# Optimization experiments

Hardware: AMD Instinct MI355X
Metric: run time of the kernel (lower is better)

The kernel has to match this reference:

```python
import jax, jax.numpy as jnp
import numpy as np

N, E, F, H, L, G, EMB, C = 50000, 600000, 128, 128, 4, 64, 64, 10
BN_EPS = 1e-5


def setup_inputs() -> dict:
    key = jax.random.key(0)
    k = lambda i: jax.random.fold_in(key, i)
    s = 0.05  # weight scale
    return {
        "x": jax.random.normal(k(0), (N, F), jnp.float32),
        "edge_index": jax.random.randint(k(1), (2, E), 0, N, jnp.int64),
        "batch": jnp.sort(jax.random.randint(k(2), (N,), 0, G, jnp.int64)),
        "emb": jax.random.normal(k(3), (G, EMB), jnp.float32),
        "eps": jnp.zeros((L,), jnp.float32),
        "W1": jax.random.normal(k(4), (L, F, H), jnp.float32) * s,
        "b1": jnp.zeros((L, H), jnp.float32),
        "W2": jax.random.normal(k(5), (L, H, H), jnp.float32) * s,
        "b2": jnp.zeros((L, H), jnp.float32),
        "gamma": jnp.ones((L, H), jnp.float32),
        "beta": jnp.zeros((L, H), jnp.float32),
        "lin1_w": jax.random.normal(k(6), (L * H + EMB, 2 * H), jnp.float32) * s,
        "lin1_b": jnp.zeros((2 * H,), jnp.float32),
        "lin2_w": jax.random.normal(k(7), (2 * H, H), jnp.float32) * s,
        "lin2_b": jnp.zeros((H,), jnp.float32),
        "lin4_w": jax.random.normal(k(8), (H, C), jnp.float32) * s,
        "lin4_b": jnp.zeros((C,), jnp.float32),
    }


def _gin_mlp(h, W1, b1, W2, b2, gamma, beta):
    # Linear -> ReLU -> Linear -> ReLU -> BatchNorm1d (batch stats)
    h = jax.nn.relu(h @ W1 + b1)
    h = jax.nn.relu(h @ W2 + b2)
    mean = jnp.mean(h, axis=0)
    var = jnp.var(h, axis=0)
    return (h - mean) * jax.lax.rsqrt(var + BN_EPS) * gamma + beta


def reference(x, edge_index, batch, emb, eps, W1, b1, W2, b2, gamma, beta,
              lin1_w, lin1_b, lin2_w, lin2_b, lin4_w, lin4_b):
    src, dst = edge_index[0], edge_index[1]
    xs = []
    for l in range(L):
        # GIN: MLP((1+eps)*x_i + sum_{j->i} x_j)  via gather + scatter-add
        agg = jax.ops.segment_sum(x[src], dst, num_segments=N)  # [N,H]
        x = _gin_mlp((1.0 + eps[l]) * x + agg,
                     W1[l], b1[l], W2[l], b2[l], gamma[l], beta[l])
        xs.append(x)
    h = jnp.concatenate(xs, axis=1)  # [N, L*H]
    # global mean pool per graph
    sums = jax.ops.segment_sum(h, batch, num_segments=G)  # [G, L*H]
    cnt = jax.ops.segment_sum(jnp.ones((N,), h.dtype), batch, num_segments=G)
    pooled = sums / jnp.maximum(cnt, 1.0)[:, None]
    z = jnp.concatenate([pooled, emb.reshape(G, -1)], axis=1)
    z = jax.nn.relu(z @ lin1_w + lin1_b)  # .relu() twice is idempotent
    # dropout p=0.5 skipped (eval mode); lin3 unused in original forward
    z = jax.nn.relu(z @ lin2_w + lin2_b)
    z = z @ lin4_w + lin4_b
    return jax.nn.log_softmax(z, axis=1)
```

## Files before the change

kernel.cpp:

```cpp
#include <hip/hip_runtime.h>
#include <cstdint>
#include <cstddef>

#define N_NODES 50000
#define N_EDGES 600000
#define NLAYER  4
#define NGRAPH  64
#define SCAN_NB 196
#define NBLK_MLP ((N_NODES + 127) / 128)
#define RED_B    ((NBLK_MLP + 12) / 13)

typedef unsigned int   u32;
typedef unsigned short u16;
typedef float f32x4  __attribute__((ext_vector_type(4)));
typedef short bf16x8 __attribute__((ext_vector_type(8)));

__device__ __forceinline__ float bf1(u16 u)  { return __uint_as_float(((u32)u) << 16); }
__device__ __forceinline__ float bflo(u32 u) { return __uint_as_float(u << 16); }
__device__ __forceinline__ float bfhi(u32 u) { return __uint_as_float(u & 0xffff0000u); }
__device__ __forceinline__ u16 f2bf(float f) {
    u32 x = __float_as_uint(f);
    u32 r = x + 0x7fffu + ((x >> 16) & 1u);
    return (u16)(r >> 16);
}
__device__ __forceinline__ u32 pack2(float a, float b) {
    return (u32)f2bf(a) | ((u32)f2bf(b) << 16);
}

__global__ __launch_bounds__(256) void cvt_x(const float2* __restrict__ x,
                                             u32* __restrict__ xbf) {
    int i = blockIdx.x * 256 + threadIdx.x;
    if (i < N_NODES * 64) { float2 v = x[i]; xbf[i] = pack2(v.x, v.y); }
}

__global__ __launch_bounds__(128) void cvt_w(const float* __restrict__ W1,
                                             const float* __restrict__ W2,
                                             short* __restrict__ W1t,
                                             short* __restrict__ W2t) {
    int l = blockIdx.y, n = blockIdx.x, k = threadIdx.x;
    const float* W = blockIdx.z ? W2 : W1;
    short* Wt      = blockIdx.z ? W2t : W1t;
    Wt[((size_t)l * 128 + n) * 128 + k] = (short)f2bf(W[((size_t)l * 128 + k) * 128 + n]);
}

__global__ void count_deg(const int* __restrict__ dst, int* __restrict__ deg) {
    int e = blockIdx.x * 256 + threadIdx.x;
    if (e < N_EDGES) atomicAdd(&deg[dst[e]], 1);
}

__global__ __launch_bounds__(256) void scan_l1(const int* __restrict__ deg,
                                               int* __restrict__ bscan,
                                               int* __restrict__ bsum) {
    __shared__ int sd[256];
    int tid = threadIdx.x;
    int i = blockIdx.x * 256 + tid;
    int v = (i < N_NODES) ? deg[i] : 0;
    sd[tid] = v; __syncthreads();
#pragma unroll
    for (int off = 1; off < 256; off <<= 1) {
        int t = (tid >= off) ? sd[tid - off] : 0;
        __syncthreads();
        sd[tid] += t; __syncthreads();
    }
    if (i < N_NODES) bscan[i] = sd[tid];
    if (tid == 255) bsum[blockIdx.x] = sd[255];
}

__global__ __launch_bounds__(256) void scan_l2(const int* __restrict__ bsum,
                                               int* __restrict__ boff) {
    __shared__ int sd[256];
    int tid = threadIdx.x;
    int v = (tid < SCAN_NB) ? bsum[tid] : 0;
    sd[tid] = v; __syncthreads();
#pragma unroll
    for (int off = 1; off < 256; off <<= 1) {
        int t = (tid >= off) ? sd[tid - off] : 0;
        __syncthreads();
        sd[tid] += t; __syncthreads();
    }
    if (tid < SCAN_NB) boff[tid] = sd[tid] - v;
}

__global__ __launch_bounds__(256) void scan_l3(const int* __restrict__ bscan,
                                               const int* __restrict__ boff,
                                               int* __restrict__ rowp) {
    int i = blockIdx.x * 256 + threadIdx.x;
    if (i == 0) rowp[0] = 0;
    if (i < N_NODES) rowp[i + 1] = bscan[i] + boff[blockIdx.x];
}

__global__ void fill_csr(const int* __restrict__ src, const int* __restrict__ dst,
                         const int* __restrict__ rowp, int* __restrict__ cursor,
                         int* __restrict__ col) {
    int e = blockIdx.x * 256 + threadIdx.x;
    if (e < N_EDGES) {
        int d = dst[e];
        int pos = atomicAdd(&cursor[d], 1);
        col[rowp[d] + pos] = src[e];
    }
}

__global__ __launch_bounds__(256) void agg_kernel(
    const u32* __restrict__ xin, const float* __restrict__ coef,
    const int* __restrict__ rowp, const int* __restrict__ col,
    const float* __restrict__ eps_all, int layer,
    u32* __restrict__ agg) {
    int node = blockIdx.x * 4 + (threadIdx.x >> 6);
    int lane = threadIdx.x & 63;
    if (node >= N_NODES) return;
    float a0 = 1.f, a1 = 1.f, d0 = 0.f, d1 = 0.f;
    if (coef) {
        a0 = coef[2 * lane];       a1 = coef[2 * lane + 1];
        d0 = coef[128 + 2 * lane]; d1 = coef[128 + 2 * lane + 1];
    }
    float ep = 1.0f + eps_all[layer];
    u32 v = xin[(size_t)node * 64 + lane];
    int k0 = rowp[node], k1 = rowp[node + 1];
    float s0 = 0.f, s1 = 0.f;
    int k = k0;
    int cc[8];
    if (k < k1) {
#pragma unroll
        for (int t = 0; t < 8; t++) cc[t] = col[min(k + t, k1 - 1)];
    }
    while (k < k1) {
        int idx[8];
#pragma unroll
        for (int t = 0; t < 8; t++) idx[t] = cc[t];
        int kn = k + 8;
        if (kn < k1) {
#pragma unroll
            for (int t = 0; t < 8; t++) cc[t] = col[min(kn + t, k1 - 1)];
        }
#pragma unroll
        for (int t = 0; t < 8; t++) {
            u32 u = xin[(size_t)idx[t] * 64 + lane];
            float w = (k + t < k1) ? 1.f : 0.f;
            s0 += w * bflo(u); s1 += w * bfhi(u);
        }
        k = kn;
    }
    float deg = (float)(k1 - k0);
    float r0 = ep * (a0 * bflo(v) + d0) + a0 * s0 + deg * d0;
    float r1 = ep * (a1 * bfhi(v) + d1) + a1 * s1 + deg * d1;
    agg[(size_t)node * 64 + lane] = pack2(r0, r1);
}

#define H1_STRIDE 136
__global__ __launch_bounds__(256) void mlp_fused(
    const short* __restrict__ A,
    const short* __restrict__ W1t, const float* __restrict__ b1,
    const short* __restrict__ W2t, const float* __restrict__ b2,
    short* __restrict__ H2, const int* __restrict__ batch,
    float* __restrict__ partial, float* __restrict__ gsum, int M) {
    __shared__ alignas(16) short h1s[128 * H1_STRIDE];
    __shared__ int sh_ga, sh_gb, sh_split;
    int tid  = threadIdx.x;
    int wave = tid >> 6, lane = tid & 63;
    int ln15 = lane & 15, quad = lane >> 4;
    int m0blk = blockIdx.x * 128;
    int m0 = m0blk + wave * 32;
    const bf16x8 zz = {0, 0, 0, 0, 0, 0, 0, 0};

    if (tid == 0) {
        int rlo = m0blk, rhi = min(m0blk + 127, M - 1);
        int ga = batch[rlo], gb = batch[rhi];
        int split = m0blk + 128;
        if (ga != gb) {
            int lo = rlo, hi = rhi;
            while (lo + 1 < hi) { int mid = (lo + hi) >> 1; if (batch[mid] == ga) lo = mid; else hi = mid; }
            split = hi;
        }
        sh_ga = ga; sh_gb = gb; sh_split = split;
    }

    bf16x8 a[2][4];
#pragma unroll
    for (int rt = 0; rt < 2; rt++) {
        int row = m0 + rt * 16 + ln15;
        const short* rp = A + (size_t)row * 128 + quad * 8;
        bool ok = row < M;
#pragma unroll
        for (int s = 0; s < 4; s++)
            a[rt][s] = ok ? *(const bf16x8*)(rp + s * 32) : zz;
    }
#pragma unroll
    for (int ct = 0; ct < 8; ct++) {
        const short* wp = W1t + (size_t)(ct * 16 + ln15) * 128 + quad * 8;
        bf16x8 b[4];
#pragma unroll
        for (int s = 0; s < 4; s++) b[s] = *(const bf16x8*)(wp + s * 32);
        float bias = b1[ct * 16 + ln15];
#pragma unroll
        for (int rt = 0; rt < 2; rt++) {
            f32x4 acc = {0.f, 0.f, 0.f, 0.f};
#pragma unroll
            for (int s = 0; s < 4; s++)
                acc = __builtin_amdgcn_mfma_f32_16x16x32_bf16(a[rt][s], b[s], acc, 0, 0, 0);
#pragma unroll
            for (int i = 0; i < 4; i++) {
                float v = fmaxf(acc[i] + bias, 0.f);
                int lr = wave * 32 + rt * 16 + quad * 4 + i;
                h1s[lr * H1_STRIDE + ct * 16 + ln15] = (short)f2bf(v);
            }
        }
    }
    __syncthreads();
    bf16x8 c[2][4];
#pragma unroll
    for (int rt = 0; rt < 2; rt++) {
        const short* rp = h1s + (size_t)(wave * 32 + rt * 16 + ln15) * H1_STRIDE + quad * 8;
#pragma unroll
        for (int s = 0; s < 4; s++) c[rt][s] = *(const bf16x8*)(rp + s * 32);
    }
    int gsplit = sh_split;
    float sAcc[8], qAcc[8], pAcc[8];
#pragma unroll
    for (int ct = 0; ct < 8; ct++) { sAcc[ct] = 0.f; qAcc[ct] = 0.f; pAcc[ct] = 0.f; }
#pragma unroll
    for (int ct = 0; ct < 8; ct++) {
        const short* wp = W2t + (size_t)(ct * 16 + ln15) * 128 + quad * 8;
        bf16x8 b[4];
#pragma unroll
        for (int s = 0; s < 4; s++) b[s] = *(const bf16x8*)(wp + s * 32);
        float bias = b2[ct * 16 + ln15];
#pragma unroll
        for (int rt = 0; rt < 2; rt++) {
            f32x4 acc = {0.f, 0.f, 0.f, 0.f};
#pragma unroll
            for (int s = 0; s < 4; s++)
                acc = __builtin_amdgcn_mfma_f32_16x16x32_bf16(c[rt][s], b[s], acc, 0, 0, 0);
            int colx = ct * 16 + ln15;
#pragma unroll
            for (int i = 0; i < 4; i++) {
                int row = m0 + rt * 16 + quad * 4 + i;
                float v = fmaxf(acc[i] + bias, 0.f);
                if (row < M) H2[(size_t)row * 128 + colx] = (short)f2bf(v);
                float vm = (row < M) ? v : 0.f;
                sAcc[ct] += vm; qAcc[ct] += vm * vm;
                if (row < gsplit) pAcc[ct] += vm;
            }
        }
    }
    __syncthreads();
    float* scr = (float*)h1s;
    int slice = wave * 4 + quad;
#pragma unroll
    for (int ct = 0; ct < 8; ct++) {
        int colx = ct * 16 + ln15;
        scr[(0 * 16 + slice) * 128 + colx] = sAcc[ct];
        scr[(1 * 16 + slice) * 128 + colx] = qAcc[ct];
        scr[(2 * 16 + slice) * 128 + colx] = pAcc[ct];
    }
    __syncthreads();
    if (tid < 128) {
        float ss = 0.f, qq = 0.f, pa = 0.f;
#pragma unroll
        for (int sl = 0; sl < 16; sl++) {
            ss += scr[(0 * 16 + sl) * 128 + tid];
            qq += scr[(1 * 16 + sl) * 128 + tid];
            pa += scr[(2 * 16 + sl) * 128 + tid];
        }
        partial[(size_t)blockIdx.x * 256 + tid]       = ss;
        partial[(size_t)blockIdx.x * 256 + 128 + tid] = qq;
        int ga = sh_ga, gb = sh_gb;
        atomicAdd(&gsum[ga * 128 + tid], pa);
        if (gb != ga) atomicAdd(&gsum[gb * 128 + tid], ss - pa);
    }
}

__global__ __launch_bounds__(256) void reduce_partials(
    const float* __restrict__ partial, float* __restrict__ sums) {
    int t = threadIdx.x;
    int b0 = blockIdx.x * 13, b1 = min(b0 + 13, NBLK_MLP);
    if (b0 >= NBLK_MLP) return;
    float acc = 0.f;
    for (int b = b0; b < b1; b++) acc += partial[(size_t)b * 256 + t];
    atomicAdd(&sums[t], acc);
}

__global__ void bn_finalize(const float* __restrict__ sums,
                            const float* __restrict__ gamma, const float* __restrict__ beta,
                            int layer, float* __restrict__ coef) {
    int c = threadIdx.x;
    float mean = sums[c] / (float)N_NODES;
    float var  = sums[128 + c] / (float)N_NODES - mean * mean;
    float istd = rsqrtf(var + 1e-5f);
    float a = istd * gamma[layer * 128 + c];
    coef[c]       = a;
    coef[128 + c] = beta[layer * 128 + c] - mean * a;
}

__global__ __launch_bounds__(256) void head_kernel(
    const float* __restrict__ gsum, const float* __restrict__ coefL,
    const int* __restrict__ batch, const float* __restrict__ emb,
    const float* __restrict__ l1w, const float* __restrict__ l1b,
    const float* __restrict__ l2w, const float* __restrict__ l2b,
    const float* __restrict__ l4w, const float* __restrict__ l4b,
    float* __restrict__ out) {
    __shared__ float z[576];
    __shared__ float z1[256];
    __shared__ float z2h[2][128];
    __shared__ float z2[128];
    __shared__ float zr[128][10];
    __shared__ float inv_cnt;
    int g = blockIdx.x;
    int tid = threadIdx.x;
    if (tid == 0) {
        int lo = 0, hi = N_NODES;
        while (lo < hi) { int m = (lo + hi) >> 1; if (batch[m] < g) lo = m + 1; else hi = m; }
        int s = lo;
        lo = 0; hi = N_NODES;
        while (lo < hi) { int m = (lo + hi) >> 1; if (batch[m] < g + 1) lo = m + 1; else hi = m; }
        inv_cnt = 1.0f / fmaxf((float)(lo - s), 1.0f);
    }
    __syncthreads();
    for (int j = tid; j < 512; j += 256) {
        int l = j >> 7, c = j & 127;
        float a = coefL[l * 256 + c], d = coefL[l * 256 + 128 + c];
        z[j] = a * gsum[(size_t)l * NGRAPH * 128 + g * 128 + c] * inv_cnt + d;
    }
    if (tid < 64) z[512 + tid] = emb[g * 64 + tid];
    __syncthreads();
    {
        float acc = l1b[tid];
        for (int j0 = 0; j0 < 576; j0 += 16) {
            float lw[16];
#pragma unroll
            for (int t = 0; t < 16; t++) lw[t] = l1w[(j0 + t) * 256 + tid];
#pragma unroll
            for (int t = 0; t < 16; t++) acc += z[j0 + t] * lw[t];
        }
        z1[tid] = fmaxf(acc, 0.f);
    }
    __syncthreads();
    {
        int c2 = tid & 127, half = tid >> 7;
        float acc = 0.f;
        int jb = half * 128;
        for (int j0 = 0; j0 < 128; j0 += 8) {
            float lw[8];
#pragma unroll
            for (int t = 0; t < 8; t++) lw[t] = l2w[(jb + j0 + t) * 128 + c2];
#pragma unroll
            for (int t = 0; t < 8; t++) acc += z1[jb + j0 + t] * lw[t];
        }
        z2h[half][c2] = acc;
    }
    __syncthreads();
    if (tid < 128) z2[tid] = fmaxf(z2h[0][tid] + z2h[1][tid] + l2b[tid], 0.f);
    __syncthreads();
    if (tid < 128) {
        float zv = z2[tid];
        const float* wr = l4w + tid * 10;
#pragma unroll
        for (int c = 0; c < 10; c++) zr[tid][c] = zv * wr[c];
    }
    __syncthreads();
    for (int s = 64; s >= 1; s >>= 1) {
        if (tid < s) {
#pragma unroll
            for (int c = 0; c < 10; c++) zr[tid][c] += zr[tid + s][c];
        }
        __syncthreads();
    }
    if (tid == 0) {
        float z3s[10];
#pragma unroll
        for (int c = 0; c < 10; c++) z3s[c] = zr[0][c] + l4b[c];
        float m = z3s[0];
        for (int i = 1; i < 10; i++) m = fmaxf(m, z3s[i]);
        float se = 0.f;
        for (int i = 0; i < 10; i++) se += expf(z3s[i] - m);
        float lse = m + logf(se);
        for (int i = 0; i < 10; i++) out[g * 10 + i] = z3s[i] - lse;
    }
}

extern "C" void kernel_launch(void* const* d_in, const int* in_sizes, int n_in,
                              void* d_out, int out_size, void* d_ws, size_t ws_size,
                              hipStream_t stream) {
    (void)in_sizes; (void)n_in; (void)out_size; (void)ws_size;
    const float* x0   = (const float*)d_in[0];
    const int* ei     = (const int*)d_in[1];
    const int* src    = ei;
    const int* dst    = ei + N_EDGES;
    const int* batch  = (const int*)d_in[2];
    const float* emb  = (const float*)d_in[3];
    const float* eps  = (const float*)d_in[4];
    const float* W1   = (const float*)d_in[5];
    const float* b1   = (const float*)d_in[6];
    const float* W2   = (const float*)d_in[7];
    const float* b2   = (const float*)d_in[8];
    const float* gamma= (const float*)d_in[9];
    const float* beta = (const float*)d_in[10];
    const float* l1w  = (const float*)d_in[11];
    const float* l1b  = (const float*)d_in[12];
    const float* l2w  = (const float*)d_in[13];
    const float* l2b  = (const float*)d_in[14];
    const float* l4w  = (const float*)d_in[15];
    const float* l4b  = (const float*)d_in[16];

    char* ws = (char*)d_ws;
    size_t off = 0;
    auto alloc = [&](size_t bytes) -> char* {
        char* p = ws + off; off += (bytes + 255) & ~(size_t)255; return p;
    };
    int* deg    = (int*)alloc(N_NODES * 4);
    int* cursor = (int*)alloc(N_NODES * 4);
    size_t zero1_len = (char*)cursor - (char*)deg + (((size_t)N_NODES * 4 + 255) & ~(size_t)255);
    int* rowp   = (int*)alloc((N_NODES + 1) * 4);
    int* bscan  = (int*)alloc(N_NODES * 4);
    int* bsum   = (int*)alloc(SCAN_NB * 4);
    int* boff   = (int*)alloc(SCAN_NB * 4);
    int* col    = (int*)alloc(N_EDGES * 4);
    u32* xbf    = (u32*)alloc((size_t)N_NODES * 64 * 4);
    u32* agg    = (u32*)alloc((size_t)N_NODES * 64 * 4);
    u32* h2a    = (u32*)alloc((size_t)N_NODES * 64 * 4);
    u32* h2b    = (u32*)alloc((size_t)N_NODES * 64 * 4);
    short* W1t  = (short*)alloc((size_t)NLAYER * 128 * 128 * 2);
    short* W2t  = (short*)alloc((size_t)NLAYER * 128 * 128 * 2);
    float* partial = (float*)alloc((size_t)NBLK_MLP * 256 * 4);
    float* sumsL = (float*)alloc(NLAYER * 256 * 4);
    float* gsumL = (float*)alloc((size_t)NLAYER * NGRAPH * 128 * 4);
    size_t zero2_len = (char*)gsumL - (char*)sumsL + (size_t)NLAYER * NGRAPH * 128 * 4;
    float* coefL = (float*)alloc(NLAYER * 256 * 4);

    hipMemsetAsync(deg, 0, zero1_len, stream);
    hipMemsetAsync(sumsL, 0, zero2_len, stream);

    cvt_x<<<(N_NODES * 64 + 255) / 256, 256, 0, stream>>>((const float2*)x0, xbf);
    {
        dim3 gw(128, NLAYER, 2);
        cvt_w<<<gw, 128, 0, stream>>>(W1, W2, W1t, W2t);
    }
    count_deg<<<(N_EDGES + 255) / 256, 256, 0, stream>>>(dst, deg);
    scan_l1<<<SCAN_NB, 256, 0, stream>>>(deg, bscan, bsum);
    scan_l2<<<1, 256, 0, stream>>>(bsum, boff);
    scan_l3<<<SCAN_NB, 256, 0, stream>>>(bscan, boff, rowp);
    fill_csr<<<(N_EDGES + 255) / 256, 256, 0, stream>>>(src, dst, rowp, cursor, col);

    const u32* xin = xbf;
    for (int l = 0; l < NLAYER; ++l) {
        u32* h2 = (l & 1) ? h2b : h2a;
        const float* coef_prev = (l == 0) ? nullptr : (coefL + (l - 1) * 256);
        agg_kernel<<<(N_NODES + 3) / 4, 256, 0, stream>>>(
            xin, coef_prev, rowp, col, eps, l, agg);
        mlp_fused<<<NBLK_MLP, 256, 0, stream>>>(
            (const short*)agg, W1t + (size_t)l * 16384, b1 + l * 128,
            W2t + (size_t)l * 16384, b2 + l * 128, (short*)h2, batch,
            partial, gsumL + (size_t)l * NGRAPH * 128, N_NODES);
        reduce_partials<<<RED_B, 256, 0, stream>>>(partial, sumsL + l * 256);
        bn_finalize<<<1, 128, 0, stream>>>(sumsL + l * 256, gamma, beta, l,
                                           coefL + l * 256);
        xin = h2;
    }
    head_kernel<<<NGRAPH, 256, 0, stream>>>(gsumL, coefL, batch, emb,
                                            l1w, l1b, l2w, l2b, l4w, l4b,
                                            (float*)d_out);
}
```

Before: 420.7 us.

## Use 512-thread MLP blocks with 16 rows per wave and merge memsets

```diff
diff --git a/kernel.cpp b/kernel.cpp
--- a/kernel.cpp
+++ b/kernel.cpp
@@ -147,7 +147,7 @@
 }
 
 #define H1_STRIDE 136
-__global__ __launch_bounds__(256) void mlp_fused(
+__global__ __launch_bounds__(512) void mlp_fused(
     const short* __restrict__ A,
     const short* __restrict__ W1t, const float* __restrict__ b1,
     const short* __restrict__ W2t, const float* __restrict__ b2,
@@ -159,7 +159,7 @@
     int wave = tid >> 6, lane = tid & 63;
     int ln15 = lane & 15, quad = lane >> 4;
     int m0blk = blockIdx.x * 128;
-    int m0 = m0blk + wave * 32;
+    int m0 = m0blk + wave * 16;
     const bf16x8 zz = {0, 0, 0, 0, 0, 0, 0, 0};
 
     if (tid == 0) {
@@ -174,15 +174,14 @@
         sh_ga = ga; sh_gb = gb; sh_split = split;
     }
 
-    bf16x8 a[2][4];
-#pragma unroll
-    for (int rt = 0; rt < 2; rt++) {
-        int row = m0 + rt * 16 + ln15;
+    bf16x8 a[4];
+    {
+        int row = m0 + ln15;
         const short* rp = A + (size_t)row * 128 + quad * 8;
         bool ok = row < M;
 #pragma unroll
         for (int s = 0; s < 4; s++)
-            a[rt][s] = ok ? *(const bf16x8*)(rp + s * 32) : zz;
+            a[s] = ok ? *(const bf16x8*)(rp + s * 32) : zz;
     }
 #pragma unroll
     for (int ct = 0; ct < 8; ct++) {
@@ -191,27 +190,23 @@
 #pragma unroll
         for (int s = 0; s < 4; s++) b[s] = *(const bf16x8*)(wp + s * 32);
         float bias = b1[ct * 16 + ln15];
-#pragma unroll
-        for (int rt = 0; rt < 2; rt++) {
-            f32x4 acc = {0.f, 0.f, 0.f, 0.f};
-#pragma unroll
-            for (int s = 0; s < 4; s++)
-                acc = __builtin_amdgcn_mfma_f32_16x16x32_bf16(a[rt][s], b[s], acc, 0, 0, 0);
-#pragma unroll
-            for (int i = 0; i < 4; i++) {
-                float v = fmaxf(acc[i] + bias, 0.f);
-                int lr = wave * 32 + rt * 16 + quad * 4 + i;
-                h1s[lr * H1_STRIDE + ct * 16 + ln15] = (short)f2bf(v);
-            }
-        }
-    }
-    __syncthreads();
-    bf16x8 c[2][4];
-#pragma unroll
-    for (int rt = 0; rt < 2; rt++) {
-        const short* rp = h1s + (size_t)(wave * 32 + rt * 16 + ln15) * H1_STRIDE + quad * 8;
-#pragma unroll
-        for (int s = 0; s < 4; s++) c[rt][s] = *(const bf16x8*)(rp + s * 32);
+        f32x4 acc = {0.f, 0.f, 0.f, 0.f};
+#pragma unroll
+        for (int s = 0; s < 4; s++)
+            acc = __builtin_amdgcn_mfma_f32_16x16x32_bf16(a[s], b[s], acc, 0, 0, 0);
+#pragma unroll
+        for (int i = 0; i < 4; i++) {
+            float v = fmaxf(acc[i] + bias, 0.f);
+            int lr = wave * 16 + quad * 4 + i;
+            h1s[lr * H1_STRIDE + ct * 16 + ln15] = (short)f2bf(v);
+        }
+    }
+    __syncthreads();
+    bf16x8 c[4];
+    {
+        const short* rp = h1s + (size_t)(wave * 16 + ln15) * H1_STRIDE + quad * 8;
+#pragma unroll
+        for (int s = 0; s < 4; s++) c[s] = *(const bf16x8*)(rp + s * 32);
     }
     int gsplit = sh_split;
     float sAcc[8], qAcc[8], pAcc[8];
@@ -224,42 +219,46 @@
 #pragma unroll
         for (int s = 0; s < 4; s++) b[s] = *(const bf16x8*)(wp + s * 32);
         float bias = b2[ct * 16 + ln15];
-#pragma unroll
-        for (int rt = 0; rt < 2; rt++) {
-            f32x4 acc = {0.f, 0.f, 0.f, 0.f};
-#pragma unroll
-            for (int s = 0; s < 4; s++)
-                acc = __builtin_amdgcn_mfma_f32_16x16x32_bf16(c[rt][s], b[s], acc, 0, 0, 0);
+        f32x4 acc = {0.f, 0.f, 0.f, 0.f};
+#pragma unroll
+        for (int s = 0; s < 4; s++)
+            acc = __builtin_amdgcn_mfma_f32_16x16x32_bf16(c[s], b[s], acc, 0, 0, 0);
+        int colx = ct * 16 + ln15;
+#pragma unroll
+        for (int i = 0; i < 4; i++) {
+            int row = m0 + quad * 4 + i;
+            float v = fmaxf(acc[i] + bias, 0.f);
+            if (row < M) H2[(size_t)row * 128 + colx] = (short)f2bf(v);
+            float vm = (row < M) ? v : 0.f;
+            sAcc[ct] += vm; qAcc[ct] += vm * vm;
+            if (row < gsplit) pAcc[ct] += vm;
+        }
+    }
+#pragma unroll
+    for (int ct = 0; ct < 8; ct++) {
+        float s = sAcc[ct]; s += __shfl_xor(s, 16, 64); s += __shfl_xor(s, 32, 64); sAcc[ct] = s;
+        float q = qAcc[ct]; q += __shfl_xor(q, 16, 64); q += __shfl_xor(q, 32, 64); qAcc[ct] = q;
+        float p = pAcc[ct]; p += __shfl_xor(p, 16, 64); p += __shfl_xor(p, 32, 64); pAcc[ct] = p;
+    }
+    __syncthreads();
+    float* scr = (float*)h1s;
+    if (quad == 0) {
+#pragma unroll
+        for (int ct = 0; ct < 8; ct++) {
             int colx = ct * 16 + ln15;
-#pragma unroll
-            for (int i = 0; i < 4; i++) {
-                int row = m0 + rt * 16 + quad * 4 + i;
-                float v = fmaxf(acc[i] + bias, 0.f);
-                if (row < M) H2[(size_t)row * 128 + colx] = (short)f2bf(v);
-                float vm = (row < M) ? v : 0.f;
-                sAcc[ct] += vm; qAcc[ct] += vm * vm;
-                if (row < gsplit) pAcc[ct] += vm;
-            }
-        }
-    }
-    __syncthreads();
-    float* scr = (float*)h1s;
-    int slice = wave * 4 + quad;
-#pragma unroll
-    for (int ct = 0; ct < 8; ct++) {
-        int colx = ct * 16 + ln15;
-        scr[(0 * 16 + slice) * 128 + colx] = sAcc[ct];
-        scr[(1 * 16 + slice) * 128 + colx] = qAcc[ct];
-        scr[(2 * 16 + slice) * 128 + colx] = pAcc[ct];
+            scr[(0 * 8 + wave) * 128 + colx] = sAcc[ct];
+            scr[(1 * 8 + wave) * 128 + colx] = qAcc[ct];
+            scr[(2 * 8 + wave) * 128 + colx] = pAcc[ct];
+        }
     }
     __syncthreads();
     if (tid < 128) {
         float ss = 0.f, qq = 0.f, pa = 0.f;
 #pragma unroll
-        for (int sl = 0; sl < 16; sl++) {
-            ss += scr[(0 * 16 + sl) * 128 + tid];
-            qq += scr[(1 * 16 + sl) * 128 + tid];
-            pa += scr[(2 * 16 + sl) * 128 + tid];
+        for (int w = 0; w < 8; w++) {
+            ss += scr[(0 * 8 + w) * 128 + tid];
+            qq += scr[(1 * 8 + w) * 128 + tid];
+            pa += scr[(2 * 8 + w) * 128 + tid];
         }
         partial[(size_t)blockIdx.x * 256 + tid]       = ss;
         partial[(size_t)blockIdx.x * 256 + 128 + tid] = qq;
@@ -408,7 +407,9 @@
     };
     int* deg    = (int*)alloc(N_NODES * 4);
     int* cursor = (int*)alloc(N_NODES * 4);
-    size_t zero1_len = (char*)cursor - (char*)deg + (((size_t)N_NODES * 4 + 255) & ~(size_t)255);
+    float* sumsL = (float*)alloc(NLAYER * 256 * 4);
+    float* gsumL = (float*)alloc((size_t)NLAYER * NGRAPH * 128 * 4);
+    size_t zero_len = (char*)gsumL - (char*)deg + (size_t)NLAYER * NGRAPH * 128 * 4;
     int* rowp   = (int*)alloc((N_NODES + 1) * 4);
     int* bscan  = (int*)alloc(N_NODES * 4);
     int* bsum   = (int*)alloc(SCAN_NB * 4);
@@ -421,13 +422,9 @@
     short* W1t  = (short*)alloc((size_t)NLAYER * 128 * 128 * 2);
     short* W2t  = (short*)alloc((size_t)NLAYER * 128 * 128 * 2);
     float* partial = (float*)alloc((size_t)NBLK_MLP * 256 * 4);
-    float* sumsL = (float*)alloc(NLAYER * 256 * 4);
-    float* gsumL = (float*)alloc((size_t)NLAYER * NGRAPH * 128 * 4);
-    size_t zero2_len = (char*)gsumL - (char*)sumsL + (size_t)NLAYER * NGRAPH * 128 * 4;
     float* coefL = (float*)alloc(NLAYER * 256 * 4);
 
-    hipMemsetAsync(deg, 0, zero1_len, stream);
-    hipMemsetAsync(sumsL, 0, zero2_len, stream);
+    hipMemsetAsync(deg, 0, zero_len, stream);
 
     cvt_x<<<(N_NODES * 64 + 255) / 256, 256, 0, stream>>>((const float2*)x0, xbf);
     {
@@ -446,7 +443,7 @@
         const float* coef_prev = (l == 0) ? nullptr : (coefL + (l - 1) * 256);
         agg_kernel<<<(N_NODES + 3) / 4, 256, 0, stream>>>(
             xin, coef_prev, rowp, col, eps, l, agg);
-        mlp_fused<<<NBLK_MLP, 256, 0, stream>>>(
+        mlp_fused<<<NBLK_MLP, 512, 0, stream>>>(
             (const short*)agg, W1t + (size_t)l * 16384, b1 + l * 128,
             W2t + (size_t)l * 16384, b2 + l * 128, (short*)h2, batch,
             partial, gsumL + (size_t)l * NGRAPH * 128, N_NODES);
```

Result: slower. 473.6 us (+12.6%).
